# Kernel optimization log

Hardware: AMD Instinct MI355X
Metric: run time of the kernel (lower is better)

Reference implementation:

```python
import jax, jax.numpy as jnp
import numpy as np

N_NODES = 100000
N_EDGES = 640000
D = 128
EPS = 1e-5

def _full_layer_norm(x):
    # torch layer_norm with normalized_shape == x.shape: stats over ALL elements
    mu = jnp.mean(x)
    var = jnp.mean(jnp.square(x - mu))  # biased variance
    return (x - mu) * jax.lax.rsqrt(var + EPS)

def setup_inputs() -> dict:
    key = jax.random.key(0)
    k1, k2, k3, k4, k5 = jax.random.split(key, 5)
    scale1 = 1.0 / np.sqrt(D)
    scale2 = 1.0 / np.sqrt(2 * D)
    return {
        "edge_features": jax.random.normal(k1, (N_EDGES, D), dtype=jnp.float32),
        "node_features": jax.random.normal(k2, (N_NODES, D), dtype=jnp.float32),
        "edge_indices": jax.random.randint(k3, (N_EDGES, 2), 0, N_NODES, dtype=jnp.int32),
        "W1": jax.random.normal(k4, (D, D), dtype=jnp.float32) * scale1,
        "b1": jnp.zeros((D,), dtype=jnp.float32),
        "W2": jax.random.normal(k5, (2 * D, D), dtype=jnp.float32) * scale2,
        "b2": jnp.zeros((D,), dtype=jnp.float32),
    }

def reference(edge_features, node_features, edge_indices, W1, b1, W2, b2):
    # node MLP: linear -> whole-tensor layernorm -> gelu
    h = node_features @ W1 + b1                       # [N, D]
    h = jax.nn.gelu(_full_layer_norm(h), approximate=False)
    # gather source-node features onto edges
    src = edge_indices[:, 0]
    dst = edge_indices[:, 1]
    gathered = h[src]                                 # [E, D]
    e = jnp.concatenate([edge_features, gathered], axis=1)  # [E, 2D]
    e = e @ W2 + b2                                   # [E, D]
    e = jax.nn.gelu(_full_layer_norm(e), approximate=False)
    # scatter-mean (include_self=False): nodes with no in-edges stay 0
    seg_sum = jax.ops.segment_sum(e, dst, num_segments=N_NODES)       # [N, D]
    counts = jax.ops.segment_sum(jnp.ones((e.shape[0],), e.dtype), dst,
                                 num_segments=N_NODES)                 # [N]
    counts = counts[:, None]
    return jnp.where(counts > 0, seg_sum / jnp.maximum(counts, 1.0), 0.0)
```

## Files before the change

kernel.cpp:

```cpp
#include <hip/hip_runtime.h>
#include <hip/hip_bf16.h>
#include <math.h>

typedef __bf16 bf16;
typedef bf16 bf16x8 __attribute__((ext_vector_type(8)));
typedef float f32x4 __attribute__((ext_vector_type(4)));
typedef unsigned short ushort_t;
typedef unsigned long long u64;

#define N_NODES 100000
#define N_EDGES 640000
#define DD 128
#define MAXDEG 64
#define STAT_SCALE 1048576.0

__device__ __forceinline__ float gelu_fast(float x) {
    float z2 = x * (1.595769122f + 0.071354816f * x * x);
    return x * __builtin_amdgcn_rcpf(1.0f + __expf(-z2));
}

__device__ __forceinline__ ushort_t bf16_bits(float x) {
    bf16 h = (bf16)x;
    return __builtin_bit_cast(ushort_t, h);
}

__device__ __forceinline__ float bits_to_f(ushort_t u) {
    return __uint_as_float(((unsigned)u) << 16);
}

__device__ __forceinline__ long long to_fixed(double x) {
    return (long long)(x * STAT_SCALE + (x >= 0.0 ? 0.5 : -0.5));
}

__device__ __forceinline__ void stats_atomic(float lsum, float lsq, float* red,
                                             u64* dsum, u64* dsq) {
    int tid = threadIdx.x;
    red[tid] = lsum; __syncthreads();
    for (int s = 128; s > 0; s >>= 1) { if (tid < s) red[tid] += red[tid + s]; __syncthreads(); }
    float bs = red[0]; __syncthreads();
    red[tid] = lsq; __syncthreads();
    for (int s = 128; s > 0; s >>= 1) { if (tid < s) red[tid] += red[tid + s]; __syncthreads(); }
    if (tid == 0) {
        atomicAdd(dsum, (u64)to_fixed((double)bs));
        atomicAdd(dsq,  (u64)to_fixed((double)red[0]));
    }
}

__device__ __forceinline__ void stats_decode(const u64* stats, double cnt,
                                             float* mu, float* rs) {
    long long ss = (long long)stats[0], sq = (long long)stats[1];
    double mu_d = ((double)ss / STAT_SCALE) / cnt;
    double var  = ((double)sq / STAT_SCALE) / cnt - mu_d * mu_d;
    *mu = (float)mu_d;
    *rs = (float)(1.0 / sqrt(var + 1e-5));
}

#define PACK8(dstp, a, b) { \
    ushort_t o_[8] = {bf16_bits(a.x), bf16_bits(a.y), bf16_bits(a.z), bf16_bits(a.w), \
                      bf16_bits(b.x), bf16_bits(b.y), bf16_bits(b.z), bf16_bits(b.w)}; \
    *(uint4*)(dstp) = *(const uint4*)o_; }

__global__ __launch_bounds__(256) void k0_init(int* __restrict__ cnt,
                                               u64* __restrict__ stats)
{
    int i = blockIdx.x * 256 + threadIdx.x;
    if (i < N_NODES) cnt[i] = 0;
    if (i < 4) stats[i] = 0ull;
}

#define K1_TILES 1563
__global__ __launch_bounds__(256) void k1_gemm1(
    const float* __restrict__ nf, const float* __restrict__ W1,
    const float* __restrict__ b1, ushort_t* __restrict__ hpre,
    u64* __restrict__ stats, int nblocks)
{
    __shared__ bf16 Ash[64 * 136];
    __shared__ float red[256];
    const int tid = threadIdx.x;
    const int lane = tid & 63;
    const int w = tid >> 6;
    const int l15 = lane & 15, l4 = lane >> 4;

    bf16x8 bfrag[4][2];
    #pragma unroll
    for (int s = 0; s < 4; ++s)
        #pragma unroll
        for (int t = 0; t < 2; ++t) {
            int n = w * 32 + t * 16 + l15;
            #pragma unroll
            for (int j = 0; j < 8; ++j)
                bfrag[s][t][j] = (bf16)W1[(s * 32 + l4 * 8 + j) * DD + n];
        }
    float4 bias4[2];
    bias4[0] = *(const float4*)&b1[w * 32 + l4 * 4];
    bias4[1] = *(const float4*)&b1[w * 32 + 16 + l4 * 4];

    float lsum = 0.f, lsq = 0.f;
    const int srow = tid >> 2;
    const int q = tid & 3;

    float4 efr[8];
    {
        int grow = min(blockIdx.x * 64 + srow, N_NODES - 1);
        const float4* p = (const float4*)&nf[(size_t)grow * DD + q * 32];
        #pragma unroll
        for (int u = 0; u < 8; ++u) efr[u] = p[u];
    }

    for (int tile = blockIdx.x; tile < K1_TILES; tile += nblocks) {
        const int rbase = tile * 64;
        __syncthreads();
        #pragma unroll
        for (int u = 0; u < 4; ++u)
            PACK8(&Ash[srow * 136 + q * 32 + u * 8], efr[2 * u], efr[2 * u + 1]);
        __syncthreads();
        int nt = tile + nblocks;
        if (nt < K1_TILES) {
            int grow = min(nt * 64 + srow, N_NODES - 1);
            const float4* p = (const float4*)&nf[(size_t)grow * DD + q * 32];
            #pragma unroll
            for (int u = 0; u < 8; ++u) efr[u] = p[u];
        }
        f32x4 acc[4][2];
        #pragma unroll
        for (int r = 0; r < 4; ++r)
            #pragma unroll
            for (int t = 0; t < 2; ++t)
                acc[r][t] = (f32x4){0.f, 0.f, 0.f, 0.f};
        #pragma unroll
        for (int s = 0; s < 4; ++s)
            #pragma unroll
            for (int r = 0; r < 4; ++r) {
                bf16x8 a = *(const bf16x8*)&Ash[(r * 16 + l15) * 136 + s * 32 + l4 * 8];
                acc[r][0] = __builtin_amdgcn_mfma_f32_16x16x32_bf16(bfrag[s][0], a, acc[r][0], 0, 0, 0);
                acc[r][1] = __builtin_amdgcn_mfma_f32_16x16x32_bf16(bfrag[s][1], a, acc[r][1], 0, 0, 0);
            }
        #pragma unroll
        for (int r = 0; r < 4; ++r) {
            int row = rbase + r * 16 + l15;
            if (row < N_NODES) {
                #pragma unroll
                for (int t = 0; t < 2; ++t) {
                    int col = w * 32 + t * 16 + l4 * 4;
                    ushort_t o[4];
                    #pragma unroll
                    for (int j = 0; j < 4; ++j) {
                        float v = acc[r][t][j] + bias4[t][j];
                        lsum += v; lsq += v * v;
                        o[j] = bf16_bits(v);
                    }
                    *(uint2*)&hpre[(size_t)row * DD + col] = *(const uint2*)o;
                }
            }
        }
    }
    stats_atomic(lsum, lsq, red, &stats[0], &stats[1]);
}

__global__ __launch_bounds__(256) void k2b_gemmh(
    const ushort_t* __restrict__ hpre, const float* __restrict__ W2,
    const float* __restrict__ b2, const u64* __restrict__ stats,
    ushort_t* __restrict__ hh, int nblocks)
{
    __shared__ bf16 Ash[64 * 136];
    float mu, rs;
    stats_decode(stats, (double)N_NODES * DD, &mu, &rs);

    const int tid = threadIdx.x;
    const int lane = tid & 63;
    const int w = tid >> 6;
    const int l15 = lane & 15, l4 = lane >> 4;

    bf16x8 bfrag[4][2];
    #pragma unroll
    for (int s = 0; s < 4; ++s)
        #pragma unroll
        for (int t = 0; t < 2; ++t) {
            int n = w * 32 + t * 16 + l15;
            #pragma unroll
            for (int j = 0; j < 8; ++j)
                bfrag[s][t][j] = (bf16)W2[(DD + s * 32 + l4 * 8 + j) * DD + n];
        }
    float4 bias4[2];
    bias4[0] = *(const float4*)&b2[w * 32 + l4 * 4];
    bias4[1] = *(const float4*)&b2[w * 32 + 16 + l4 * 4];

    const int srow = tid >> 2;
    const int q = tid & 3;

    uint4 hr[4];
    {
        int grow = min(blockIdx.x * 64 + srow, N_NODES - 1);
        const uint4* p = (const uint4*)&hpre[(size_t)grow * DD + q * 32];
        #pragma unroll
        for (int u = 0; u < 4; ++u) hr[u] = p[u];
    }

    for (int tile = blockIdx.x; tile < K1_TILES; tile += nblocks) {
        const int rbase = tile * 64;
        __syncthreads();
        #pragma unroll
        for (int u = 0; u < 4; ++u) {
            const ushort_t* in = (const ushort_t*)&hr[u];
            ushort_t o[8];
            #pragma unroll
            for (int j = 0; j < 8; ++j)
                o[j] = bf16_bits(gelu_fast((bits_to_f(in[j]) - mu) * rs));
            *(uint4*)&Ash[srow * 136 + q * 32 + u * 8] = *(const uint4*)o;
        }
        __syncthreads();
        int nt = tile + nblocks;
        if (nt < K1_TILES) {
            int grow = min(nt * 64 + srow, N_NODES - 1);
            const uint4* p = (const uint4*)&hpre[(size_t)grow * DD + q * 32];
            #pragma unroll
            for (int u = 0; u < 4; ++u) hr[u] = p[u];
        }
        f32x4 acc[4][2];
        #pragma unroll
        for (int r = 0; r < 4; ++r)
            #pragma unroll
            for (int t = 0; t < 2; ++t)
                acc[r][t] = (f32x4){0.f, 0.f, 0.f, 0.f};
        #pragma unroll
        for (int s = 0; s < 4; ++s)
            #pragma unroll
            for (int r = 0; r < 4; ++r) {
                bf16x8 a = *(const bf16x8*)&Ash[(r * 16 + l15) * 136 + s * 32 + l4 * 8];
                acc[r][0] = __builtin_amdgcn_mfma_f32_16x16x32_bf16(bfrag[s][0], a, acc[r][0], 0, 0, 0);
                acc[r][1] = __builtin_amdgcn_mfma_f32_16x16x32_bf16(bfrag[s][1], a, acc[r][1], 0, 0, 0);
            }
        #pragma unroll
        for (int r = 0; r < 4; ++r) {
            int row = rbase + r * 16 + l15;
            if (row < N_NODES) {
                #pragma unroll
                for (int t = 0; t < 2; ++t) {
                    int col = w * 32 + t * 16 + l4 * 4;
                    ushort_t o[4];
                    #pragma unroll
                    for (int j = 0; j < 4; ++j)
                        o[j] = bf16_bits(acc[r][t][j] + bias4[t][j]);
                    *(uint2*)&hh[(size_t)row * DD + col] = *(const uint2*)o;
                }
            }
        }
    }
}

#define K4_WTILES (N_EDGES / 16)
__global__ __launch_bounds__(256) void k4_gemm2(
    const float* __restrict__ ef, const ushort_t* __restrict__ hh,
    const int* __restrict__ eidx, const float* __restrict__ W2,
    ushort_t* __restrict__ e0, u64* __restrict__ stats, int nblocks)
{
    __shared__ bf16 Bsh[128 * 136];
    __shared__ float red[256];
    const int tid = threadIdx.x;
    const int lane = tid & 63;
    const int w = tid >> 6;
    const int l15 = lane & 15, l4 = lane >> 4;

    if (tid < 128) {
        int n = tid;
        #pragma unroll
        for (int kb = 0; kb < 16; ++kb) {
            float v[8];
            #pragma unroll
            for (int j = 0; j < 8; ++j)
                v[j] = W2[(size_t)(kb * 8 + j) * DD + n];
            ushort_t o[8];
            #pragma unroll
            for (int j = 0; j < 8; ++j) o[j] = bf16_bits(v[j]);
            *(uint4*)&Bsh[n * 136 + kb * 8] = *(const uint4*)o;
        }
    }
    __syncthreads();

    float lsum = 0.f, lsq = 0.f;

    for (int g = blockIdx.x * 4 + w; g < K4_WTILES; g += nblocks * 4) {
        const int row = g * 16 + l15;
        int src = eidx[(size_t)row * 2];
        float4 a0[4], a1[4];
        #pragma unroll
        for (int s = 0; s < 4; ++s) {
            const float4* pa = (const float4*)&ef[(size_t)row * DD + s * 32 + l4 * 8];
            a0[s] = pa[0]; a1[s] = pa[1];
        }
        uint2 hv[8];
        #pragma unroll
        for (int t = 0; t < 8; ++t)
            hv[t] = *(const uint2*)&hh[(size_t)src * DD + t * 16 + l4 * 4];

        f32x4 acc[8];
        #pragma unroll
        for (int t = 0; t < 8; ++t) acc[t] = (f32x4){0.f, 0.f, 0.f, 0.f};

        #pragma unroll
        for (int s = 0; s < 4; ++s) {
            ushort_t af[8] = {bf16_bits(a0[s].x), bf16_bits(a0[s].y), bf16_bits(a0[s].z), bf16_bits(a0[s].w),
                              bf16_bits(a1[s].x), bf16_bits(a1[s].y), bf16_bits(a1[s].z), bf16_bits(a1[s].w)};
            bf16x8 afrag = *(const bf16x8*)af;
            #pragma unroll
            for (int t = 0; t < 8; ++t) {
                bf16x8 bfrag = *(const bf16x8*)&Bsh[(t * 16 + l15) * 136 + s * 32 + l4 * 8];
                acc[t] = __builtin_amdgcn_mfma_f32_16x16x32_bf16(bfrag, afrag, acc[t], 0, 0, 0);
            }
        }

        #pragma unroll
        for (int t = 0; t < 8; ++t) {
            float hadd[4] = {bits_to_f((ushort_t)(hv[t].x & 0xffff)),
                             bits_to_f((ushort_t)(hv[t].x >> 16)),
                             bits_to_f((ushort_t)(hv[t].y & 0xffff)),
                             bits_to_f((ushort_t)(hv[t].y >> 16))};
            ushort_t o[4];
            #pragma unroll
            for (int j = 0; j < 4; ++j) {
                float v = acc[t][j] + hadd[j];
                lsum += v; lsq += v * v;
                o[j] = bf16_bits(v);
            }
            *(uint2*)&e0[(size_t)row * DD + t * 16 + l4 * 4] = *(const uint2*)o;
        }
    }
    stats_atomic(lsum, lsq, red, &stats[2], &stats[3]);
}

__global__ __launch_bounds__(256) void k7_fill(
    const int* __restrict__ eidx, int* __restrict__ cnt, int* __restrict__ slot)
{
    int e = blockIdx.x * 256 + threadIdx.x;
    if (e >= N_EDGES) return;
    int dst = eidx[(size_t)e * 2 + 1];
    int pos = atomicAdd(&cnt[dst], 1);
    if (pos < MAXDEG) slot[dst * MAXDEG + pos] = e;
}

__global__ __launch_bounds__(256) void k8_gather(
    const ushort_t* __restrict__ e0v, const int* __restrict__ slot,
    const int* __restrict__ cnt, const u64* __restrict__ stats,
    float* __restrict__ out)
{
    float mu, rs;
    stats_decode(stats + 2, (double)N_EDGES * DD, &mu, &rs);
    int node = (int)((blockIdx.x * 256 + threadIdx.x) >> 6);
    int lane = threadIdx.x & 63;
    if (node >= N_NODES) return;
    const int hl = lane >> 5;
    const int l31 = lane & 31;
    int c = cnt[node];
    int m = min(c, MAXDEG);
    int myslot = (lane < m) ? slot[node * MAXDEG + lane] : 0;
    float a0 = 0.f, a1 = 0.f, a2 = 0.f, a3 = 0.f;
    const size_t off = (size_t)(l31 * 4);

    int steps = m >> 1;
    int s = 0;
    for (; s + 2 <= steps; s += 2) {
        int eA = __shfl(myslot, 2 * s + hl);
        int eB = __shfl(myslot, 2 * (s + 1) + hl);
        uint2 uA = *(const uint2*)&e0v[(size_t)eA * DD + off];
        uint2 uB = *(const uint2*)&e0v[(size_t)eB * DD + off];
        a0 += gelu_fast((__uint_as_float(uA.x << 16) - mu) * rs);
        a1 += gelu_fast((__uint_as_float(uA.x & 0xffff0000u) - mu) * rs);
        a2 += gelu_fast((__uint_as_float(uA.y << 16) - mu) * rs);
        a3 += gelu_fast((__uint_as_float(uA.y & 0xffff0000u) - mu) * rs);
        a0 += gelu_fast((__uint_as_float(uB.x << 16) - mu) * rs);
        a1 += gelu_fast((__uint_as_float(uB.x & 0xffff0000u) - mu) * rs);
        a2 += gelu_fast((__uint_as_float(uB.y << 16) - mu) * rs);
        a3 += gelu_fast((__uint_as_float(uB.y & 0xffff0000u) - mu) * rs);
    }
    for (; s < steps; ++s) {
        int eA = __shfl(myslot, 2 * s + hl);
        uint2 uA = *(const uint2*)&e0v[(size_t)eA * DD + off];
        a0 += gelu_fast((__uint_as_float(uA.x << 16) - mu) * rs);
        a1 += gelu_fast((__uint_as_float(uA.x & 0xffff0000u) - mu) * rs);
        a2 += gelu_fast((__uint_as_float(uA.y << 16) - mu) * rs);
        a3 += gelu_fast((__uint_as_float(uA.y & 0xffff0000u) - mu) * rs);
    }
    if (m & 1) {
        int eA = __shfl(myslot, m - 1);
        uint2 uA = *(const uint2*)&e0v[(size_t)eA * DD + off];
        float g0 = gelu_fast((__uint_as_float(uA.x << 16) - mu) * rs);
        float g1 = gelu_fast((__uint_as_float(uA.x & 0xffff0000u) - mu) * rs);
        float g2 = gelu_fast((__uint_as_float(uA.y << 16) - mu) * rs);
        float g3 = gelu_fast((__uint_as_float(uA.y & 0xffff0000u) - mu) * rs);
        if (hl == 0) { a0 += g0; a1 += g1; a2 += g2; a3 += g3; }
    }
    a0 += __shfl_xor(a0, 32);
    a1 += __shfl_xor(a1, 32);
    a2 += __shfl_xor(a2, 32);
    a3 += __shfl_xor(a3, 32);
    if (hl == 0) {
        float inv = c > 0 ? 1.0f / (float)c : 0.f;
        float4 res = {a0 * inv, a1 * inv, a2 * inv, a3 * inv};
        *(float4*)&out[(size_t)node * DD + l31 * 4] = res;
    }
}

extern "C" void kernel_launch(void* const* d_in, const int* in_sizes, int n_in,
                              void* d_out, int out_size, void* d_ws, size_t ws_size,
                              hipStream_t stream) {
    const float* ef  = (const float*)d_in[0];
    const float* nf  = (const float*)d_in[1];
    const int*   eix = (const int*)d_in[2];
    const float* W1  = (const float*)d_in[3];
    const float* b1  = (const float*)d_in[4];
    const float* W2  = (const float*)d_in[5];
    const float* b2  = (const float*)d_in[6];
    float* out = (float*)d_out;
    char* ws = (char*)d_ws;

    ushort_t* hpre  = (ushort_t*)(ws + 0);
    ushort_t* hh    = (ushort_t*)(ws + 25600000);
    ushort_t* e0    = (ushort_t*)(ws + 51200000);
    int*      cnt   = (int*)(ws + 215040000);
    u64*      stats = (u64*)(ws + 215440000);
    int*      slot  = (int*)(ws + 215440064);

    k0_init<<<391, 256, 0, stream>>>(cnt, stats);
    k7_fill<<<2500, 256, 0, stream>>>(eix, cnt, slot);
    k1_gemm1<<<782, 256, 0, stream>>>(nf, W1, b1, hpre, stats, 782);
    k2b_gemmh<<<782, 256, 0, stream>>>(hpre, W2, b2, stats, hh, 782);
    k4_gemm2<<<2500, 256, 0, stream>>>(ef, hh, eix, W2, e0, stats, 2500);
    k8_gather<<<25000, 256, 0, stream>>>(e0, slot, cnt, stats, out);
}
```

Measured before the change: 322.5 us.

## Software-pipeline edge GEMM loads and double-buffer LDS in node GEMMs

The edge GEMM kernel now runs as a persistent loop on fewer blocks. It prefetches the next tile's edge-feature panel, the next source index two tiles ahead, and the gathered node row into register sets that alternate, so global load latency overlaps the MFMA work. The two node GEMM kernels double-buffer their shared-memory A tile, which removes one barrier per iteration. W2 staging into LDS is also spread across all 256 threads. The cost is higher register pressure from the duplicated prefetch buffers, which may lower occupancy.

```diff
diff --git a/kernel.cpp b/kernel.cpp
--- a/kernel.cpp
+++ b/kernel.cpp
@@ -74,7 +74,7 @@
     const float* __restrict__ b1, ushort_t* __restrict__ hpre,
     u64* __restrict__ stats, int nblocks)
 {
-    __shared__ bf16 Ash[64 * 136];
+    __shared__ bf16 Ash[2][64 * 136];
     __shared__ float red[256];
     const int tid = threadIdx.x;
     const int lane = tid & 63;
@@ -107,12 +107,12 @@
         for (int u = 0; u < 8; ++u) efr[u] = p[u];
     }
 
+    int buf = 0;
     for (int tile = blockIdx.x; tile < K1_TILES; tile += nblocks) {
         const int rbase = tile * 64;
-        __syncthreads();
         #pragma unroll
         for (int u = 0; u < 4; ++u)
-            PACK8(&Ash[srow * 136 + q * 32 + u * 8], efr[2 * u], efr[2 * u + 1]);
+            PACK8(&Ash[buf][srow * 136 + q * 32 + u * 8], efr[2 * u], efr[2 * u + 1]);
         __syncthreads();
         int nt = tile + nblocks;
         if (nt < K1_TILES) {
@@ -131,7 +131,7 @@
         for (int s = 0; s < 4; ++s)
             #pragma unroll
             for (int r = 0; r < 4; ++r) {
-                bf16x8 a = *(const bf16x8*)&Ash[(r * 16 + l15) * 136 + s * 32 + l4 * 8];
+                bf16x8 a = *(const bf16x8*)&Ash[buf][(r * 16 + l15) * 136 + s * 32 + l4 * 8];
                 acc[r][0] = __builtin_amdgcn_mfma_f32_16x16x32_bf16(bfrag[s][0], a, acc[r][0], 0, 0, 0);
                 acc[r][1] = __builtin_amdgcn_mfma_f32_16x16x32_bf16(bfrag[s][1], a, acc[r][1], 0, 0, 0);
             }
@@ -153,6 +153,7 @@
                 }
             }
         }
+        buf ^= 1;
     }
     stats_atomic(lsum, lsq, red, &stats[0], &stats[1]);
 }
@@ -162,7 +163,7 @@
     const float* __restrict__ b2, const u64* __restrict__ stats,
     ushort_t* __restrict__ hh, int nblocks)
 {
-    __shared__ bf16 Ash[64 * 136];
+    __shared__ bf16 Ash[2][64 * 136];
     float mu, rs;
     stats_decode(stats, (double)N_NODES * DD, &mu, &rs);
 
@@ -196,9 +197,9 @@
         for (int u = 0; u < 4; ++u) hr[u] = p[u];
     }
 
+    int buf = 0;
     for (int tile = blockIdx.x; tile < K1_TILES; tile += nblocks) {
         const int rbase = tile * 64;
-        __syncthreads();
         #pragma unroll
         for (int u = 0; u < 4; ++u) {
             const ushort_t* in = (const ushort_t*)&hr[u];
@@ -206,7 +207,7 @@
             #pragma unroll
             for (int j = 0; j < 8; ++j)
                 o[j] = bf16_bits(gelu_fast((bits_to_f(in[j]) - mu) * rs));
-            *(uint4*)&Ash[srow * 136 + q * 32 + u * 8] = *(const uint4*)o;
+            *(uint4*)&Ash[buf][srow * 136 + q * 32 + u * 8] = *(const uint4*)o;
         }
         __syncthreads();
         int nt = tile + nblocks;
@@ -226,7 +227,7 @@
         for (int s = 0; s < 4; ++s)
             #pragma unroll
             for (int r = 0; r < 4; ++r) {
-                bf16x8 a = *(const bf16x8*)&Ash[(r * 16 + l15) * 136 + s * 32 + l4 * 8];
+                bf16x8 a = *(const bf16x8*)&Ash[buf][(r * 16 + l15) * 136 + s * 32 + l4 * 8];
                 acc[r][0] = __builtin_amdgcn_mfma_f32_16x16x32_bf16(bfrag[s][0], a, acc[r][0], 0, 0, 0);
                 acc[r][1] = __builtin_amdgcn_mfma_f32_16x16x32_bf16(bfrag[s][1], a, acc[r][1], 0, 0, 0);
             }
@@ -245,10 +246,61 @@
                 }
             }
         }
+        buf ^= 1;
     }
 }
 
 #define K4_WTILES (N_EDGES / 16)
+
+#define K4_LOAD_SRC(dst, t) { if ((t) < K4_WTILES) dst = eidx[(size_t)((t) * 16 + l15) * 2]; }
+
+#define K4_LOAD_PANEL(raw, t) { if ((t) < K4_WTILES) { \
+    const float* base_ = &ef[(size_t)((t) * 16 + l15) * DD + l4 * 8]; \
+    raw##0 = *(const float4*)(base_);       raw##1 = *(const float4*)(base_ + 4); \
+    raw##2 = *(const float4*)(base_ + 32);  raw##3 = *(const float4*)(base_ + 36); \
+    raw##4 = *(const float4*)(base_ + 64);  raw##5 = *(const float4*)(base_ + 68); \
+    raw##6 = *(const float4*)(base_ + 96);  raw##7 = *(const float4*)(base_ + 100); } }
+
+#define K4_LOAD_HV(hv, srcreg, t) { if ((t) < K4_WTILES) { \
+    const ushort_t* hb_ = &hh[(size_t)(srcreg) * DD + l4 * 4]; \
+    hv[0] = *(const uint2*)(hb_);       hv[1] = *(const uint2*)(hb_ + 16); \
+    hv[2] = *(const uint2*)(hb_ + 32);  hv[3] = *(const uint2*)(hb_ + 48); \
+    hv[4] = *(const uint2*)(hb_ + 64);  hv[5] = *(const uint2*)(hb_ + 80); \
+    hv[6] = *(const uint2*)(hb_ + 96);  hv[7] = *(const uint2*)(hb_ + 112); } }
+
+#define K4_COMPUTE_STORE(t, raw, hv) { \
+    f32x4 acc[8]; \
+    _Pragma("unroll") \
+    for (int tt = 0; tt < 8; ++tt) acc[tt] = (f32x4){0.f, 0.f, 0.f, 0.f}; \
+    _Pragma("unroll") \
+    for (int s = 0; s < 4; ++s) { \
+        float4 ra_ = raw##_arr(2 * s), rb_ = raw##_arr(2 * s + 1); \
+        ushort_t af_[8] = {bf16_bits(ra_.x), bf16_bits(ra_.y), bf16_bits(ra_.z), bf16_bits(ra_.w), \
+                           bf16_bits(rb_.x), bf16_bits(rb_.y), bf16_bits(rb_.z), bf16_bits(rb_.w)}; \
+        bf16x8 afrag = *(const bf16x8*)af_; \
+        _Pragma("unroll") \
+        for (int tt = 0; tt < 8; ++tt) { \
+            bf16x8 bfr = *(const bf16x8*)&Bsh[(tt * 16 + l15) * 136 + s * 32 + l4 * 8]; \
+            acc[tt] = __builtin_amdgcn_mfma_f32_16x16x32_bf16(bfr, afrag, acc[tt], 0, 0, 0); \
+        } \
+    } \
+    const int row_ = (t) * 16 + l15; \
+    _Pragma("unroll") \
+    for (int tt = 0; tt < 8; ++tt) { \
+        float hadd_[4] = {bits_to_f((ushort_t)(hv[tt].x & 0xffff)), \
+                          bits_to_f((ushort_t)(hv[tt].x >> 16)), \
+                          bits_to_f((ushort_t)(hv[tt].y & 0xffff)), \
+                          bits_to_f((ushort_t)(hv[tt].y >> 16))}; \
+        ushort_t o_[4]; \
+        _Pragma("unroll") \
+        for (int j = 0; j < 4; ++j) { \
+            float v_ = acc[tt][j] + hadd_[j]; \
+            lsum += v_; lsq += v_ * v_; \
+            o_[j] = bf16_bits(v_); \
+        } \
+        *(uint2*)&e0[(size_t)row_ * DD + tt * 16 + l4 * 4] = *(const uint2*)o_; \
+    } }
+
 __global__ __launch_bounds__(256) void k4_gemm2(
     const float* __restrict__ ef, const ushort_t* __restrict__ hh,
     const int* __restrict__ eidx, const float* __restrict__ W2,
@@ -261,69 +313,53 @@
     const int w = tid >> 6;
     const int l15 = lane & 15, l4 = lane >> 4;
 
-    if (tid < 128) {
-        int n = tid;
-        #pragma unroll
-        for (int kb = 0; kb < 16; ++kb) {
-            float v[8];
+    {
+        int n = tid & 127;
+        int kb0 = (tid >> 7) * 8;
+        #pragma unroll
+        for (int i = 0; i < 8; ++i) {
+            int kb = kb0 + i;
+            ushort_t o[8];
             #pragma unroll
             for (int j = 0; j < 8; ++j)
-                v[j] = W2[(size_t)(kb * 8 + j) * DD + n];
-            ushort_t o[8];
-            #pragma unroll
-            for (int j = 0; j < 8; ++j) o[j] = bf16_bits(v[j]);
+                o[j] = bf16_bits(W2[(size_t)(kb * 8 + j) * DD + n]);
             *(uint4*)&Bsh[n * 136 + kb * 8] = *(const uint4*)o;
         }
     }
     __syncthreads();
 
     float lsum = 0.f, lsq = 0.f;
-
-    for (int g = blockIdx.x * 4 + w; g < K4_WTILES; g += nblocks * 4) {
-        const int row = g * 16 + l15;
-        int src = eidx[(size_t)row * 2];
-        float4 a0[4], a1[4];
-        #pragma unroll
-        for (int s = 0; s < 4; ++s) {
-            const float4* pa = (const float4*)&ef[(size_t)row * DD + s * 32 + l4 * 8];
-            a0[s] = pa[0]; a1[s] = pa[1];
-        }
-        uint2 hv[8];
-        #pragma unroll
-        for (int t = 0; t < 8; ++t)
-            hv[t] = *(const uint2*)&hh[(size_t)src * DD + t * 16 + l4 * 4];
-
-        f32x4 acc[8];
-        #pragma unroll
-        for (int t = 0; t < 8; ++t) acc[t] = (f32x4){0.f, 0.f, 0.f, 0.f};
-
-        #pragma unroll
-        for (int s = 0; s < 4; ++s) {
-            ushort_t af[8] = {bf16_bits(a0[s].x), bf16_bits(a0[s].y), bf16_bits(a0[s].z), bf16_bits(a0[s].w),
-                              bf16_bits(a1[s].x), bf16_bits(a1[s].y), bf16_bits(a1[s].z), bf16_bits(a1[s].w)};
-            bf16x8 afrag = *(const bf16x8*)af;
-            #pragma unroll
-            for (int t = 0; t < 8; ++t) {
-                bf16x8 bfrag = *(const bf16x8*)&Bsh[(t * 16 + l15) * 136 + s * 32 + l4 * 8];
-                acc[t] = __builtin_amdgcn_mfma_f32_16x16x32_bf16(bfrag, afrag, acc[t], 0, 0, 0);
-            }
-        }
-
-        #pragma unroll
-        for (int t = 0; t < 8; ++t) {
-            float hadd[4] = {bits_to_f((ushort_t)(hv[t].x & 0xffff)),
-                             bits_to_f((ushort_t)(hv[t].x >> 16)),
-                             bits_to_f((ushort_t)(hv[t].y & 0xffff)),
-                             bits_to_f((ushort_t)(hv[t].y >> 16))};
-            ushort_t o[4];
-            #pragma unroll
-            for (int j = 0; j < 4; ++j) {
-                float v = acc[t][j] + hadd[j];
-                lsum += v; lsq += v * v;
-                o[j] = bf16_bits(v);
-            }
-            *(uint2*)&e0[(size_t)row * DD + t * 16 + l4 * 4] = *(const uint2*)o;
-        }
+    const int S = nblocks * 4;
+
+    float4 rA0, rA1, rA2, rA3, rA4, rA5, rA6, rA7;
+    float4 rB0, rB1, rB2, rB3, rB4, rB5, rB6, rB7;
+    #define rA_arr(i) (i==0?rA0:i==1?rA1:i==2?rA2:i==3?rA3:i==4?rA4:i==5?rA5:i==6?rA6:rA7)
+    #define rB_arr(i) (i==0?rB0:i==1?rB1:i==2?rB2:i==3?rB3:i==4?rB4:i==5?rB5:i==6?rB6:rB7)
+    uint2 hvA[8], hvB[8];
+    int srcA = 0, srcB = 0, srcC = 0;
+
+    int g = blockIdx.x * 4 + w;
+    K4_LOAD_SRC(srcA, g);
+    K4_LOAD_PANEL(rA, g);
+    K4_LOAD_SRC(srcB, g + S);
+    K4_LOAD_HV(hvA, srcA, g);
+
+    while (g < K4_WTILES) {
+        {
+            K4_LOAD_SRC(srcC, g + 2 * S);
+            K4_LOAD_HV(hvB, srcB, g + S);
+            K4_LOAD_PANEL(rB, g + S);
+            K4_COMPUTE_STORE(g, rA, hvA);
+        }
+        g += S;
+        if (g >= K4_WTILES) break;
+        {
+            K4_LOAD_SRC(srcB, g + 2 * S);
+            K4_LOAD_HV(hvA, srcC, g + S);
+            K4_LOAD_PANEL(rA, g + S);
+            K4_COMPUTE_STORE(g, rB, hvB);
+        }
+        g += S;
     }
     stats_atomic(lsum, lsq, red, &stats[2], &stats[3]);
 }
@@ -424,6 +460,6 @@
     k7_fill<<<2500, 256, 0, stream>>>(eix, cnt, slot);
     k1_gemm1<<<782, 256, 0, stream>>>(nf, W1, b1, hpre, stats, 782);
     k2b_gemmh<<<782, 256, 0, stream>>>(hpre, W2, b2, stats, hh, 782);
-    k4_gemm2<<<2500, 256, 0, stream>>>(ef, hh, eix, W2, e0, stats, 2500);
+    k4_gemm2<<<1024, 256, 0, stream>>>(ef, hh, eix, W2, e0, stats, 1024);
     k8_gather<<<25000, 256, 0, stream>>>(e0, slot, cnt, stats, out);
 }
```

Measured after the change: 298.7 us. 7.4% less time.
